# Optimization experiments

Measured on AMD Instinct MI355X. Metric: run time of the kernel, lower is better.

The kernel has to match this reference:

```python
import jax, jax.numpy as jnp
import numpy as np

INPUT_DIM, HIDDEN, OUTPUT_DIM, NUM_LAYERS = 512, 128, 96, 5
BATCH, SEQ = 64, 512


def _gru_layer(x_seq, w_ih, w_hh, b_ih, b_hh):
    """Single GRU layer, PyTorch gate conventions. x_seq: [B,T,I] -> [B,T,H]."""
    B = x_seq.shape[0]
    H = w_hh.shape[1]
    # Precompute input-to-hidden gates for all timesteps: [B,T,3H]
    gx = jnp.einsum('bti,gi->btg', x_seq, w_ih) + b_ih

    def step(h, gx_t):
        gh = h @ w_hh.T + b_hh                      # [B,3H]
        xr, xz, xn = jnp.split(gx_t, 3, axis=-1)
        hr, hz, hn = jnp.split(gh, 3, axis=-1)
        r = jax.nn.sigmoid(xr + hr)
        z = jax.nn.sigmoid(xz + hz)
        n = jnp.tanh(xn + r * hn)
        h_new = (1.0 - z) * n + z * h
        return h_new, h_new

    h0 = jnp.zeros((B, H), x_seq.dtype)
    _, hs = jax.lax.scan(step, h0, jnp.swapaxes(gx, 0, 1))  # [T,B,H]
    return jnp.swapaxes(hs, 0, 1)                           # [B,T,H]


def setup_inputs() -> dict:
    key = jax.random.key(0)
    ks = jax.random.split(key, 8)
    s = 1.0 / np.sqrt(HIDDEN)  # torch default uniform init bound
    u = lambda k, shape: jax.random.uniform(k, shape, jnp.float32, -s, s)
    return {
        'x': jax.random.normal(ks[0], (BATCH, SEQ, INPUT_DIM), jnp.float32),
        'w_ih0': u(ks[1], (3 * HIDDEN, INPUT_DIM)),
        'w_ih_rest': u(ks[2], (NUM_LAYERS - 1, 3 * HIDDEN, HIDDEN)),
        'w_hh': u(ks[3], (NUM_LAYERS, 3 * HIDDEN, HIDDEN)),
        'b_ih': u(ks[4], (NUM_LAYERS, 3 * HIDDEN)),
        'b_hh': u(ks[5], (NUM_LAYERS, 3 * HIDDEN)),
        'fc_w': u(ks[6], (OUTPUT_DIM, HIDDEN)),
        'fc_b': u(ks[7], (OUTPUT_DIM,)),
    }


def reference(x, w_ih0, w_ih_rest, w_hh, b_ih, b_hh, fc_w, fc_b):
    h = _gru_layer(x, w_ih0, w_hh[0], b_ih[0], b_hh[0])
    for l in range(1, NUM_LAYERS):
        h = _gru_layer(h, w_ih_rest[l - 1], w_hh[l], b_ih[l], b_hh[l])
    # final linear on last timestep: [B,H] -> [B,OUTPUT_DIM]
    return h[:, -1, :] @ fc_w.T + fc_b
```

## Files before the change

### kernel.cpp

```cpp
#include <hip/hip_runtime.h>
#include <hip/hip_bf16.h>

#define BATCH   64
#define SEQ     512
#define IN0     512
#define HID     128
#define G3      384
#define NLAY    5
#define CHUNK   8

typedef _Float16 f16x8 __attribute__((ext_vector_type(8)));
typedef float    f32x4 __attribute__((ext_vector_type(4)));

static __device__ __forceinline__ float sigf(float x) {
    return __builtin_amdgcn_rcpf(1.f + __expf(-x));
}
static __device__ __forceinline__ float tanh_fast(float x) {
    const float e = exp2f(fabsf(x) * -2.885390082f);
    return copysignf((1.f - e) * __builtin_amdgcn_rcpf(1.f + e), x);
}

__global__ __launch_bounds__(256) void gemm_gx(const float* __restrict__ A,
                                               const float* __restrict__ W,
                                               const float* __restrict__ bias,
                                               float* __restrict__ gx)
{
    __shared__ __align__(16) _Float16 As[64][40];
    __shared__ __align__(16) _Float16 Bs[64][40];

    const int tid  = threadIdx.x;
    const int lane = tid & 63;
    const int wv   = tid >> 6;
    const int n16  = lane & 15;
    const int quad = lane >> 4;
    const int row0 = blockIdx.x * 64;
    const int col0 = blockIdx.y * 64;
    const int r    = tid >> 2;
    const int kc   = (tid & 3) * 8;

    f32x4 acc[4];
    #pragma unroll
    for (int nt = 0; nt < 4; nt++) acc[nt] = (f32x4){0.f, 0.f, 0.f, 0.f};

    for (int k0 = 0; k0 < IN0; k0 += 32) {
        {
            const float* Ap = A + (size_t)(row0 + r) * IN0 + k0 + kc;
            float4 a0 = *(const float4*)(Ap);
            float4 a1 = *(const float4*)(Ap + 4);
            f16x8 v;
            v[0] = (_Float16)a0.x; v[1] = (_Float16)a0.y; v[2] = (_Float16)a0.z; v[3] = (_Float16)a0.w;
            v[4] = (_Float16)a1.x; v[5] = (_Float16)a1.y; v[6] = (_Float16)a1.z; v[7] = (_Float16)a1.w;
            *(f16x8*)&As[r][kc] = v;
        }
        {
            const float* Wp = W + (size_t)(col0 + r) * IN0 + k0 + kc;
            float4 b0 = *(const float4*)(Wp);
            float4 b1 = *(const float4*)(Wp + 4);
            f16x8 v;
            v[0] = (_Float16)b0.x; v[1] = (_Float16)b0.y; v[2] = (_Float16)b0.z; v[3] = (_Float16)b0.w;
            v[4] = (_Float16)b1.x; v[5] = (_Float16)b1.y; v[6] = (_Float16)b1.z; v[7] = (_Float16)b1.w;
            *(f16x8*)&Bs[r][kc] = v;
        }
        __syncthreads();

        const f16x8 af = *(const f16x8*)&As[wv * 16 + n16][quad * 8];
        #pragma unroll
        for (int nt = 0; nt < 4; nt++) {
            const f16x8 bfr = *(const f16x8*)&Bs[nt * 16 + n16][quad * 8];
            acc[nt] = __builtin_amdgcn_mfma_f32_16x16x32_f16(af, bfr, acc[nt], 0, 0, 0);
        }
        __syncthreads();
    }

    #pragma unroll
    for (int nt = 0; nt < 4; nt++) {
        const int col = col0 + nt * 16 + n16;
        const float bb = bias[col];
        #pragma unroll
        for (int r4 = 0; r4 < 4; r4++) {
            const int row = row0 + wv * 16 + quad * 4 + r4;
            gx[(size_t)row * G3 + col] = acc[nt][r4] + bb;
        }
    }
}

__global__ __launch_bounds__(512, 2) void gru_pipeline(
    const float* __restrict__ gx0,
    const float* __restrict__ w_ih_rest,
    const float* __restrict__ w_hh,
    const float* __restrict__ b_ih,
    const float* __restrict__ b_hh,
    _Float16* __restrict__ hmid,
    float* __restrict__ hlast,
    int* __restrict__ flags)
{
    const int l    = blockIdx.x >> 2;
    const int g    = blockIdx.x & 3;
    const int bm0  = g * 16;
    const int tid  = threadIdx.x;
    const int lane = tid & 63;
    const int n16  = lane & 15;
    const int quad = lane >> 4;
    const int wv   = tid >> 6;
    const int j    = wv * 16 + n16;

    __shared__ __align__(16) _Float16 hS[CHUNK][16][136];
    __shared__ __align__(16) int bslots[8];

    f16x8 bf[3][4];
    {
        const float* wb = w_hh + (size_t)l * G3 * HID;
        #pragma unroll
        for (int tau = 0; tau < 3; tau++)
            #pragma unroll
            for (int kc = 0; kc < 4; kc++) {
                const float* wp = wb + (size_t)(tau * 128 + j) * HID + kc * 32 + quad * 8;
                f16x8 v;
                #pragma unroll
                for (int i = 0; i < 8; i++) v[i] = (_Float16)wp[i];
                bf[tau][kc] = v;
            }
    }
    f16x8 bi[3][4];
    if (l > 0) {
        const float* wb = w_ih_rest + (size_t)(l - 1) * G3 * HID;
        #pragma unroll
        for (int tau = 0; tau < 3; tau++)
            #pragma unroll
            for (int kc = 0; kc < 4; kc++) {
                const float* wp = wb + (size_t)(tau * 128 + j) * HID + kc * 32 + quad * 8;
                f16x8 v;
                #pragma unroll
                for (int i = 0; i < 8; i++) v[i] = (_Float16)wp[i];
                bi[tau][kc] = v;
            }
    }
    const float bcr = b_hh[l * G3 + j]       + ((l > 0) ? b_ih[l * G3 + j]       : 0.f);
    const float bcz = b_hh[l * G3 + j + 128] + ((l > 0) ? b_ih[l * G3 + j + 128] : 0.f);
    const float bcn = b_hh[l * G3 + j + 256];
    const float bxn = (l > 0) ? b_ih[l * G3 + j + 256] : 0.f;

    for (int i = tid; i < CHUNK * 16 * 136; i += 512) ((_Float16*)hS)[i] = (_Float16)0.f;
    float vhp[4] = {0.f, 0.f, 0.f, 0.f};
    if (tid < 8) bslots[tid] = 0;

    const float* pR[4];
    float xr[4], xz[4], xn[4];
    if (l == 0) {
        #pragma unroll
        for (int r = 0; r < 4; r++) {
            pR[r] = gx0 + (size_t)(bm0 + quad * 4 + r) * SEQ * G3 + j;
            xr[r] = pR[r][0]; xz[r] = pR[r][128]; xn[r] = pR[r][256];
            pR[r] += G3;
        }
    }

    const _Float16* hprev = (l > 0) ? hmid + (size_t)((l - 1) * 4 + g) * SEQ * 2048 : (const _Float16*)nullptr;
    _Float16*       hpub  = (l < 4) ? hmid + (size_t)(l * 4 + g) * SEQ * 2048 : (_Float16*)nullptr;
    int*       dstflag = (l < 4) ? &flags[l * 4 + g] : (int*)nullptr;
    const int* srcflag = (l > 0) ? &flags[(l - 1) * 4 + g] : (const int*)nullptr;

    f16x8 ap[4];
    const int hoff = n16 * 128 + quad * 8;

    __syncthreads();

    volatile int* vb = bslots;
    const int myslot = lane & 7;

    for (int c = 0; c < SEQ / CHUNK; c++) {
        const int t0 = c * CHUNK;

        if (l > 0) {
            const int need = t0 + CHUNK;
            int v = __hip_atomic_load(srcflag, __ATOMIC_RELAXED, __HIP_MEMORY_SCOPE_AGENT);
            while (v < need) {
                __builtin_amdgcn_s_sleep(2);
                v = __hip_atomic_load(srcflag, __ATOMIC_RELAXED, __HIP_MEMORY_SCOPE_AGENT);
            }
            (void)__hip_atomic_load(srcflag, __ATOMIC_ACQUIRE, __HIP_MEMORY_SCOPE_AGENT);
            __asm__ volatile("" ::: "memory");
            const _Float16* hp = hprev + (size_t)t0 * 2048 + hoff;
            #pragma unroll
            for (int kc = 0; kc < 4; kc++) ap[kc] = *(const f16x8*)(hp + kc * 32);
        }

        #pragma unroll
        for (int i = 0; i < CHUNK; i++) {
            const int t = t0 + i;
            const int sc = t + 1;

            __asm__ volatile("" ::: "memory");
            if (lane == 0) vb[wv] = sc;
            {
                int v;
                do { v = vb[myslot]; } while (!__all(v >= sc));
            }
            __asm__ volatile("" ::: "memory");

            const int rb = (i + CHUNK - 1) & (CHUNK - 1);
            f16x8 af[4];
            #pragma unroll
            for (int kc = 0; kc < 4; kc++)
                af[kc] = *(const f16x8*)&hS[rb][n16][kc * 32 + quad * 8];

            f32x4 ai0 = {0.f, 0.f, 0.f, 0.f}, ai1 = ai0;
            f32x4 ai2 = {bxn, bxn, bxn, bxn};
            if (l > 0) {
                #pragma unroll
                for (int kc = 0; kc < 4; kc++) {
                    ai0 = __builtin_amdgcn_mfma_f32_16x16x32_f16(ap[kc], bi[0][kc], ai0, 0, 0, 0);
                    ai1 = __builtin_amdgcn_mfma_f32_16x16x32_f16(ap[kc], bi[1][kc], ai1, 0, 0, 0);
                    ai2 = __builtin_amdgcn_mfma_f32_16x16x32_f16(ap[kc], bi[2][kc], ai2, 0, 0, 0);
                }
            }

            if (l > 0 && i < CHUNK - 1) {
                const _Float16* hp = hprev + (size_t)(t + 1) * 2048 + hoff;
                #pragma unroll
                for (int kc = 0; kc < 4; kc++) ap[kc] = *(const f16x8*)(hp + kc * 32);
            }

            float nr[4], nz[4], nn[4];
            if (l == 0) {
                #pragma unroll
                for (int r = 0; r < 4; r++) {
                    nr[r] = pR[r][0]; nz[r] = pR[r][128]; nn[r] = pR[r][256];
                }
                if (t + 1 < SEQ) {
                    #pragma unroll
                    for (int r = 0; r < 4; r++) pR[r] += G3;
                }
            }

            f32x4 ah0 = {bcr, bcr, bcr, bcr};
            f32x4 ah1 = {bcz, bcz, bcz, bcz};
            f32x4 ah2 = {bcn, bcn, bcn, bcn};
            #pragma unroll
            for (int kc = 0; kc < 4; kc++) {
                ah0 = __builtin_amdgcn_mfma_f32_16x16x32_f16(af[kc], bf[0][kc], ah0, 0, 0, 0);
                ah1 = __builtin_amdgcn_mfma_f32_16x16x32_f16(af[kc], bf[1][kc], ah1, 0, 0, 0);
                ah2 = __builtin_amdgcn_mfma_f32_16x16x32_f16(af[kc], bf[2][kc], ah2, 0, 0, 0);
            }

            #pragma unroll
            for (int r = 0; r < 4; r++) {
                const float sxr = (l == 0) ? xr[r] : ai0[r];
                const float sxz = (l == 0) ? xz[r] : ai1[r];
                const float sxn = (l == 0) ? xn[r] : ai2[r];
                const float rg  = sigf(sxr + ah0[r]);
                const float zg  = sigf(sxz + ah1[r]);
                const float th  = tanh_fast(fmaf(rg, ah2[r], sxn));
                const float hnew = fmaf(zg, vhp[r] - th, th);
                vhp[r] = hnew;
                hS[i][quad * 4 + r][j] = (_Float16)hnew;
                if (l == 4 && t == SEQ - 1)
                    hlast[(bm0 + quad * 4 + r) * 128 + j] = hnew;
            }

            if (l == 0) {
                #pragma unroll
                for (int r = 0; r < 4; r++) { xr[r] = nr[r]; xz[r] = nz[r]; xn[r] = nn[r]; }
            }
        }

        if (l < 4) {
            __syncthreads();
            _Float16* dstc = hpub + (size_t)t0 * 2048;
            {
                const int seg0 = tid;
                const int seg1 = tid + 512;
                const int seg2 = tid + 1024;
                const int seg3 = tid + 1536;
                f16x8 v0 = *(const f16x8*)&hS[(seg0 >> 8)][(seg0 >> 4) & 15][(seg0 & 15) * 8];
                f16x8 v1 = *(const f16x8*)&hS[(seg1 >> 8)][(seg1 >> 4) & 15][(seg1 & 15) * 8];
                f16x8 v2 = *(const f16x8*)&hS[(seg2 >> 8)][(seg2 >> 4) & 15][(seg2 & 15) * 8];
                f16x8 v3 = *(const f16x8*)&hS[(seg3 >> 8)][(seg3 >> 4) & 15][(seg3 & 15) * 8];
                *(f16x8*)(dstc + (seg0 >> 4) * 128 + (seg0 & 15) * 8) = v0;
                *(f16x8*)(dstc + (seg1 >> 4) * 128 + (seg1 & 15) * 8) = v1;
                *(f16x8*)(dstc + (seg2 >> 4) * 128 + (seg2 & 15) * 8) = v2;
                *(f16x8*)(dstc + (seg3 >> 4) * 128 + (seg3 & 15) * 8) = v3;
            }
            __syncthreads();
            if (tid == 0)
                __hip_atomic_store(dstflag, t0 + CHUNK, __ATOMIC_RELEASE, __HIP_MEMORY_SCOPE_AGENT);
        }
    }
}

__global__ __launch_bounds__(128) void fc_kernel(const float* __restrict__ hlast,
                                                 const float* __restrict__ fc_w,
                                                 const float* __restrict__ fc_b,
                                                 float* __restrict__ out)
{
    const int b = blockIdx.x;
    const int o = threadIdx.x;
    if (o < 96) {
        const float* h = hlast + (size_t)b * HID;
        const float* wrow = fc_w + o * HID;
        float acc = fc_b[o];
        #pragma unroll 4
        for (int k = 0; k < HID; k++) acc = fmaf(h[k], wrow[k], acc);
        out[b * 96 + o] = acc;
    }
}

extern "C" void kernel_launch(void* const* d_in, const int* in_sizes, int n_in,
                              void* d_out, int out_size, void* d_ws, size_t ws_size,
                              hipStream_t stream)
{
    const float* x         = (const float*)d_in[0];
    const float* w_ih0     = (const float*)d_in[1];
    const float* w_ih_rest = (const float*)d_in[2];
    const float* w_hh      = (const float*)d_in[3];
    const float* b_ih      = (const float*)d_in[4];
    const float* b_hh      = (const float*)d_in[5];
    const float* fc_w      = (const float*)d_in[6];
    const float* fc_b      = (const float*)d_in[7];
    float* out = (float*)d_out;

    int*      flags = (int*)d_ws;
    float*    gxbuf = (float*)((char*)d_ws + 256);
    _Float16* hmid  = (_Float16*)((char*)d_ws + 256 + 50331648);
    float*    hlast = (float*)((char*)d_ws + 256 + 50331648 + 33554432);

    hipMemsetAsync(d_ws, 0, 256, stream);

    const dim3 gemmGrid(512, 6);
    gemm_gx<<<gemmGrid, 256, 0, stream>>>(x, w_ih0, b_ih, gxbuf);

    gru_pipeline<<<NLAY * 4, 512, 0, stream>>>(gxbuf, w_ih_rest, w_hh, b_ih, b_hh,
                                               hmid, hlast, flags);

    fc_kernel<<<BATCH, 128, 0, stream>>>(hlast, fc_w, fc_b, out);
}
```

Measured before the change: 863.5 us.

## Fuse input GEMM into GRU pipeline kernel with per-window readiness flags

Merges the layer-0 input-projection GEMM into the persistent GRU kernel as 3072 extra blocks. The GEMM tiles are ordered by time window, and each tile bumps a per-(batch group, time window) counter when it finishes. Layer-0 recurrence blocks wait only on the counter for the window they need next, so the recurrence can start before the whole GEMM is done and one kernel launch boundary goes away. The trade-offs are extra spin-waiting and a dependency on the 20 recurrence blocks being resident while the GEMM blocks run, which is a deadlock risk if scheduling differs.

```diff
diff --git a/kernel.cpp b/kernel.cpp
--- a/kernel.cpp
+++ b/kernel.cpp
@@ -20,72 +20,10 @@
     return copysignf((1.f - e) * __builtin_amdgcn_rcpf(1.f + e), x);
 }
 
-__global__ __launch_bounds__(256) void gemm_gx(const float* __restrict__ A,
-                                               const float* __restrict__ W,
-                                               const float* __restrict__ bias,
-                                               float* __restrict__ gx)
-{
-    __shared__ __align__(16) _Float16 As[64][40];
-    __shared__ __align__(16) _Float16 Bs[64][40];
-
-    const int tid  = threadIdx.x;
-    const int lane = tid & 63;
-    const int wv   = tid >> 6;
-    const int n16  = lane & 15;
-    const int quad = lane >> 4;
-    const int row0 = blockIdx.x * 64;
-    const int col0 = blockIdx.y * 64;
-    const int r    = tid >> 2;
-    const int kc   = (tid & 3) * 8;
-
-    f32x4 acc[4];
-    #pragma unroll
-    for (int nt = 0; nt < 4; nt++) acc[nt] = (f32x4){0.f, 0.f, 0.f, 0.f};
-
-    for (int k0 = 0; k0 < IN0; k0 += 32) {
-        {
-            const float* Ap = A + (size_t)(row0 + r) * IN0 + k0 + kc;
-            float4 a0 = *(const float4*)(Ap);
-            float4 a1 = *(const float4*)(Ap + 4);
-            f16x8 v;
-            v[0] = (_Float16)a0.x; v[1] = (_Float16)a0.y; v[2] = (_Float16)a0.z; v[3] = (_Float16)a0.w;
-            v[4] = (_Float16)a1.x; v[5] = (_Float16)a1.y; v[6] = (_Float16)a1.z; v[7] = (_Float16)a1.w;
-            *(f16x8*)&As[r][kc] = v;
-        }
-        {
-            const float* Wp = W + (size_t)(col0 + r) * IN0 + k0 + kc;
-            float4 b0 = *(const float4*)(Wp);
-            float4 b1 = *(const float4*)(Wp + 4);
-            f16x8 v;
-            v[0] = (_Float16)b0.x; v[1] = (_Float16)b0.y; v[2] = (_Float16)b0.z; v[3] = (_Float16)b0.w;
-            v[4] = (_Float16)b1.x; v[5] = (_Float16)b1.y; v[6] = (_Float16)b1.z; v[7] = (_Float16)b1.w;
-            *(f16x8*)&Bs[r][kc] = v;
-        }
-        __syncthreads();
-
-        const f16x8 af = *(const f16x8*)&As[wv * 16 + n16][quad * 8];
-        #pragma unroll
-        for (int nt = 0; nt < 4; nt++) {
-            const f16x8 bfr = *(const f16x8*)&Bs[nt * 16 + n16][quad * 8];
-            acc[nt] = __builtin_amdgcn_mfma_f32_16x16x32_f16(af, bfr, acc[nt], 0, 0, 0);
-        }
-        __syncthreads();
-    }
-
-    #pragma unroll
-    for (int nt = 0; nt < 4; nt++) {
-        const int col = col0 + nt * 16 + n16;
-        const float bb = bias[col];
-        #pragma unroll
-        for (int r4 = 0; r4 < 4; r4++) {
-            const int row = row0 + wv * 16 + quad * 4 + r4;
-            gx[(size_t)row * G3 + col] = acc[nt][r4] + bb;
-        }
-    }
-}
-
-__global__ __launch_bounds__(512, 2) void gru_pipeline(
-    const float* __restrict__ gx0,
+__global__ __launch_bounds__(512, 2) void gru_fused(
+    const float* __restrict__ x,
+    const float* __restrict__ w_ih0,
+    float* __restrict__ gx,
     const float* __restrict__ w_ih_rest,
     const float* __restrict__ w_hh,
     const float* __restrict__ b_ih,
@@ -94,18 +32,81 @@
     float* __restrict__ hlast,
     int* __restrict__ flags)
 {
-    const int l    = blockIdx.x >> 2;
-    const int g    = blockIdx.x & 3;
-    const int bm0  = g * 16;
+    __shared__ __align__(16) char smem[34848];
+
     const int tid  = threadIdx.x;
     const int lane = tid & 63;
     const int n16  = lane & 15;
     const int quad = lane >> 4;
+
+    if (blockIdx.x >= 20) {
+        const int gi    = blockIdx.x - 20;
+        const int tslot = gi / 384;
+        const int rem   = gi % 384;
+        const int bb    = rem / 6;
+        const int nb    = rem % 6;
+        const int row0  = bb * 512 + tslot * 64;
+        const int col0  = nb * 64;
+
+        _Float16 (*As)[40] = (_Float16(*)[40])smem;
+        _Float16 (*Bs)[40] = (_Float16(*)[40])(smem + 5120);
+
+        const int wv   = tid >> 6;
+        const int msub = wv & 3;
+        const int nh   = wv >> 2;
+
+        f32x4 acc0 = {0.f, 0.f, 0.f, 0.f}, acc1 = acc0;
+
+        const int half = tid >> 8;
+        const int u    = tid & 255;
+        const int r    = u >> 2;
+        const int kc   = (u & 3) * 8;
+        const float* src0 = (half == 0)
+            ? x     + (size_t)(row0 + r) * IN0
+            : w_ih0 + (size_t)(col0 + r) * IN0;
+        _Float16* dst = (half == 0) ? &As[r][kc] : &Bs[r][kc];
+
+        for (int k0 = 0; k0 < IN0; k0 += 32) {
+            float4 a0 = *(const float4*)(src0 + k0 + kc);
+            float4 a1 = *(const float4*)(src0 + k0 + kc + 4);
+            f16x8 v;
+            v[0] = (_Float16)a0.x; v[1] = (_Float16)a0.y; v[2] = (_Float16)a0.z; v[3] = (_Float16)a0.w;
+            v[4] = (_Float16)a1.x; v[5] = (_Float16)a1.y; v[6] = (_Float16)a1.z; v[7] = (_Float16)a1.w;
+            *(f16x8*)dst = v;
+            __syncthreads();
+            const f16x8 af  = *(const f16x8*)&As[msub * 16 + n16][quad * 8];
+            const f16x8 bf0 = *(const f16x8*)&Bs[nh * 32 + n16][quad * 8];
+            const f16x8 bf1 = *(const f16x8*)&Bs[nh * 32 + 16 + n16][quad * 8];
+            acc0 = __builtin_amdgcn_mfma_f32_16x16x32_f16(af, bf0, acc0, 0, 0, 0);
+            acc1 = __builtin_amdgcn_mfma_f32_16x16x32_f16(af, bf1, acc1, 0, 0, 0);
+            __syncthreads();
+        }
+        #pragma unroll
+        for (int nt = 0; nt < 2; nt++) {
+            const f32x4 a = nt ? acc1 : acc0;
+            const int col = col0 + nh * 32 + nt * 16 + n16;
+            const float bbias = b_ih[col];
+            #pragma unroll
+            for (int r4 = 0; r4 < 4; r4++) {
+                const int row = row0 + msub * 16 + quad * 4 + r4;
+                gx[(size_t)row * G3 + col] = a[r4] + bbias;
+            }
+        }
+        __syncthreads();
+        if (tid == 0)
+            __hip_atomic_fetch_add(&flags[16 + (bb >> 4) * 8 + tslot], 1,
+                                   __ATOMIC_RELEASE, __HIP_MEMORY_SCOPE_AGENT);
+        return;
+    }
+
+    const int l    = blockIdx.x >> 2;
+    const int g    = blockIdx.x & 3;
+    const int bm0  = g * 16;
     const int wv   = tid >> 6;
     const int j    = wv * 16 + n16;
 
-    __shared__ __align__(16) _Float16 hS[CHUNK][16][136];
-    __shared__ __align__(16) int bslots[8];
+    _Float16 (*hS)[16][136] = (_Float16(*)[16][136])smem;
+    int* bslots = (int*)(smem + 34816);
 
     f16x8 bf[3][4];
     {
@@ -146,14 +147,23 @@
 
     const float* pR[4];
     float xr[4], xz[4], xn[4];
+    const int* gxw = &flags[16 + g * 8];
     if (l == 0) {
+        int v = __hip_atomic_load(&gxw[0], __ATOMIC_RELAXED, __HIP_MEMORY_SCOPE_AGENT);
+        while (v < 96) {
+            __builtin_amdgcn_s_sleep(2);
+            v = __hip_atomic_load(&gxw[0], __ATOMIC_RELAXED, __HIP_MEMORY_SCOPE_AGENT);
+        }
+        (void)__hip_atomic_load(&gxw[0], __ATOMIC_ACQUIRE, __HIP_MEMORY_SCOPE_AGENT);
+        __asm__ volatile("" ::: "memory");
         #pragma unroll
         for (int r = 0; r < 4; r++) {
-            pR[r] = gx0 + (size_t)(bm0 + quad * 4 + r) * SEQ * G3 + j;
+            pR[r] = gx + (size_t)(bm0 + quad * 4 + r) * SEQ * G3 + j;
             xr[r] = pR[r][0]; xz[r] = pR[r][128]; xn[r] = pR[r][256];
             pR[r] += G3;
         }
     }
+    int wcur = 0;
 
     const _Float16* hprev = (l > 0) ? hmid + (size_t)((l - 1) * 4 + g) * SEQ * 2048 : (const _Float16*)nullptr;
     _Float16*       hpub  = (l < 4) ? hmid + (size_t)(l * 4 + g) * SEQ * 2048 : (_Float16*)nullptr;
@@ -183,6 +193,18 @@
             const _Float16* hp = hprev + (size_t)t0 * 2048 + hoff;
             #pragma unroll
             for (int kc = 0; kc < 4; kc++) ap[kc] = *(const f16x8*)(hp + kc * 32);
+        } else {
+            int wneed = (t0 + CHUNK) >> 6; if (wneed > 7) wneed = 7;
+            if (wneed != wcur) {
+                int v = __hip_atomic_load(&gxw[wneed], __ATOMIC_RELAXED, __HIP_MEMORY_SCOPE_AGENT);
+                while (v < 96) {
+                    __builtin_amdgcn_s_sleep(2);
+                    v = __hip_atomic_load(&gxw[wneed], __ATOMIC_RELAXED, __HIP_MEMORY_SCOPE_AGENT);
+                }
+                (void)__hip_atomic_load(&gxw[wneed], __ATOMIC_ACQUIRE, __HIP_MEMORY_SCOPE_AGENT);
+                __asm__ volatile("" ::: "memory");
+                wcur = wneed;
+            }
         }
 
         #pragma unroll
@@ -326,11 +348,8 @@
 
     hipMemsetAsync(d_ws, 0, 256, stream);
 
-    const dim3 gemmGrid(512, 6);
-    gemm_gx<<<gemmGrid, 256, 0, stream>>>(x, w_ih0, b_ih, gxbuf);
-
-    gru_pipeline<<<NLAY * 4, 512, 0, stream>>>(gxbuf, w_ih_rest, w_hh, b_ih, b_hh,
-                                               hmid, hlast, flags);
+    gru_fused<<<20 + 3072, 512, 0, stream>>>(x, w_ih0, gxbuf, w_ih_rest, w_hh,
+                                             b_ih, b_hh, hmid, hlast, flags);
 
     fc_kernel<<<BATCH, 128, 0, stream>>>(hlast, fc_w, fc_b, out);
 }
```

After: 923.4 us. +6.9%, slower.
